# Kernel tuning notes

Measured on AMD Instinct MI355X. Metric: run time of the kernel, lower is better.

The kernel has to match this reference:

```python
import jax, jax.numpy as jnp
import numpy as np

BUCKET_BINS = np.array([0, 1, 2, 3, 4, 5, 7, 8, 15, 16, 31, 32, 63, 64], dtype=np.int32)
MAX_WINDOW = 8  # args.span_maximum_length


def _span_index_table(L):
    # Static enumeration of all spans of width 1..MAX_WINDOW (stride-1 unfold).
    starts, ends = [], []
    for w in range(1, min(L, MAX_WINDOW) + 1):
        s = np.arange(0, L - w + 1)
        starts.append(s)
        ends.append(s + w)
    return (np.concatenate(starts).astype(np.int32),
            np.concatenate(ends).astype(np.int32))


def _bucket(width):
    # index of last bin with width >= bin value
    return jnp.searchsorted(jnp.asarray(BUCKET_BINS), width, side='right') - 1


def _fnn(h, W1, b1, W2, b2, W3, b3):
    # Linear->ReLU->(Dropout: eval identity)->Linear->ReLU->Linear->Softmax
    h = jax.nn.relu(h @ W1 + b1)
    h = jax.nn.relu(h @ W2 + b2)
    return jax.nn.softmax(h @ W3 + b3, axis=-1)


def setup_inputs() -> dict:
    key = jax.random.key(0)
    ks = jax.random.split(key, 16)
    B, L, D = 8, 256, 768
    H, WD, DD = 1024, 25, 25
    span_dim = 2 * D + WD          # 1561
    pair_dim = 2 * span_dim + DD   # 3147
    f = jnp.float32

    def g(k, shape, scale):
        return jax.random.normal(k, shape, dtype=f) * scale

    return {
        'x': g(ks[0], (B, L, D), 1.0),
        'width_emb': g(ks[1], (len(BUCKET_BINS), WD), 0.02),
        'dist_emb': g(ks[2], (len(BUCKET_BINS), DD), 0.02),
        'Ws1': g(ks[3], (span_dim, H), 0.02), 'bs1': jnp.zeros((H,), f),
        'Ws2': g(ks[4], (H, H), 0.02), 'bs2': jnp.zeros((H,), f),
        'Ws3': g(ks[5], (H, 3), 0.02), 'bs3': jnp.zeros((3,), f),
        'Wp1': g(ks[6], (pair_dim, H), 0.02), 'bp1': jnp.zeros((H,), f),
        'Wp2': g(ks[7], (H, H), 0.02), 'bp2': jnp.zeros((H,), f),
        'Wp3': g(ks[8], (H, 4), 0.02), 'bp3': jnp.zeros((4,), f),
        'nz': 64,
    }


def reference(x, width_emb, dist_emb, Ws1, bs1, Ws2, bs2, Ws3, bs3,
              Wp1, bp1, Wp2, bp2, Wp3, bp3, nz):
    B, L, D = x.shape
    starts_np, ends_np = _span_index_table(L)
    starts = jnp.asarray(starts_np)
    ends = jnp.asarray(ends_np)

    # ---- SpanRepresentation: [start token, end token, width bucket emb] ----
    w_emb = width_emb[_bucket(ends - starts)]                     # [S, WD]
    spans = jnp.concatenate([
        x[:, starts_np, :],                                       # [B,S,D]
        x[:, ends_np - 1, :],                                     # [B,S,D]
        jnp.broadcast_to(w_emb, (B,) + w_emb.shape),              # [B,S,WD]
    ], axis=-1)                                                   # [B,S,span_dim]

    # ---- span_fnn + PrunedTargetOpinion (top-k on aspect/opinion probs) ----
    span_prob = _fnn(spans, Ws1, bs1, Ws2, bs2, Ws3, bs3)         # [B,S,3]
    _, t_idx = jax.lax.top_k(span_prob[:, :, 1], nz)              # aspect  [B,nz]
    _, o_idx = jax.lax.top_k(span_prob[:, :, 2], nz)              # opinion [B,nz]

    # ---- PairRepresentation: all target x opinion pairs ----
    t_rep = jnp.take_along_axis(spans, t_idx[:, :, None], axis=1) # [B,nz,sd]
    o_rep = jnp.take_along_axis(spans, o_idx[:, :, None], axis=1)
    ta, tb = starts[t_idx], ends[t_idx]                           # [B,nz]
    oc, od = starts[o_idx], ends[o_idx]
    # min_distance(a,b,c,d) = min(|b-c|, |a-d|)
    dist = jnp.minimum(jnp.abs(tb[:, :, None] - oc[:, None, :]),
                       jnp.abs(ta[:, :, None] - od[:, None, :]))  # [B,nz,nz]
    d_emb = dist_emb[_bucket(dist)]                               # [B,nz,nz,DD]
    sd = spans.shape[-1]
    pairs = jnp.concatenate([
        jnp.broadcast_to(t_rep[:, :, None, :], (B, nz, nz, sd)),
        jnp.broadcast_to(o_rep[:, None, :, :], (B, nz, nz, sd)),
        d_emb,
    ], axis=-1).reshape(B, nz * nz, 2 * sd + d_emb.shape[-1])     # [B,nz^2,pair_dim]

    pair_prob = _fnn(pairs, Wp1, bp1, Wp2, bp2, Wp3, bp3)         # [B,nz^2,4]
    return span_prob, pair_prob
```

## Files before the change

### kernel.cpp

```cpp
#include <hip/hip_runtime.h>
#include <cstdint>
#include <cstddef>

#define BATCH 8
#define SEQ   256
#define DIM   768
#define NSPAN 2020
#define HID   1024
#define NZ    64

typedef unsigned short u16;
typedef unsigned int   u32;
typedef unsigned long long u64;

typedef __bf16 bf16x8 __attribute__((ext_vector_type(8)));
typedef float  f32x4  __attribute__((ext_vector_type(4)));

__device__ __forceinline__ u16 f2bf(float f) {
    union { float f; u32 u; } x; x.f = f;
    u32 r = x.u + 0x7fffu + ((x.u >> 16) & 1u);
    return (u16)(r >> 16);
}
__device__ __forceinline__ float bf2f(u16 b) {
    union { u32 u; float f; } x; x.u = ((u32)b) << 16;
    return x.f;
}
__device__ __forceinline__ void splitbf(float v, u16& h, u16& l) {
    h = f2bf(v);
    l = f2bf(v - bf2f(h));
}

__device__ __forceinline__ void gld_lds16(const void* g, void* l) {
    __builtin_amdgcn_global_load_lds(
        (const __attribute__((address_space(1))) unsigned int*)g,
        (__attribute__((address_space(3))) unsigned int*)l, 16, 0, 0);
}

__device__ __forceinline__ void span_decode(int s, int& start, int& end, int& w) {
    int off = 0;
#pragma unroll
    for (int wi = 1; wi <= 8; ++wi) {
        int cnt = SEQ - wi + 1;
        if (s < off + cnt) { w = wi; start = s - off; end = start + wi; return; }
        off += cnt;
    }
    w = 8; start = 0; end = 8;
}

__device__ __forceinline__ int dbucket(int d) {
    int b = 0;
    b += (d >= 1);  b += (d >= 2);  b += (d >= 3);  b += (d >= 4);
    b += (d >= 5);  b += (d >= 7);  b += (d >= 8);  b += (d >= 15);
    b += (d >= 16); b += (d >= 31); b += (d >= 32); b += (d >= 63);
    b += (d >= 64);
    return b;
}

__device__ __forceinline__ void xcd_map(int L, int sft, int& bx, int& by) {
    int grp = L >> (3 + sft);
    int rem = L & ((1 << (3 + sft)) - 1);
    bx = rem >> 3;
    by = (grp << 3) | (rem & 7);
}

__global__ __launch_bounds__(256) void k_prep(
    const float* __restrict__ x,  u16* __restrict__ xh,   u16* __restrict__ xl,
    const float* __restrict__ wemb, const float* __restrict__ demb,
    const float* __restrict__ Ws1, const float* __restrict__ bs1,
    const float* __restrict__ Wp1, const float* __restrict__ bp1,
    float* __restrict__ wtabS, float* __restrict__ wtabPt,
    float* __restrict__ wtabPo, float* __restrict__ dtab)
{
    int bid = blockIdx.x, tid = threadIdx.x;
    if (bid < 6144) {
        int i = bid * 256 + tid;
        u16 h, l; splitbf(x[i], h, l);
        xh[i] = h; xl[i] = l;
        return;
    }
    int t = bid - 6144;
    int row = t >> 2;
    int h = (t & 3) * 256 + tid;
    const int wb[8] = {1,2,3,4,5,5,6,7};
    if (row < 8) {
        int bk = wb[row];
        float acc = bs1[h];
        for (int j = 0; j < 25; ++j) acc = fmaf(wemb[bk*25+j], Ws1[(size_t)(1536+j)*HID + h], acc);
        wtabS[row*HID + h] = acc;
    } else if (row < 16) {
        int bk = wb[row-8];
        float acc = 0.f;
        for (int j = 0; j < 25; ++j) acc = fmaf(wemb[bk*25+j], Wp1[(size_t)(1536+j)*HID + h], acc);
        wtabPt[(row-8)*HID + h] = acc;
    } else if (row < 24) {
        int bk = wb[row-16];
        float acc = 0.f;
        for (int j = 0; j < 25; ++j) acc = fmaf(wemb[bk*25+j], Wp1[(size_t)(3097+j)*HID + h], acc);
        wtabPo[(row-16)*HID + h] = acc;
    } else {
        int tt = row - 24;
        float acc = bp1[h];
        for (int j = 0; j < 25; ++j) acc = fmaf(demb[tt*25+j], Wp1[(size_t)(3122+j)*HID + h], acc);
        dtab[tt*HID + h] = acc;
    }
}

__global__ __launch_bounds__(256) void k_transpose(
    const float* __restrict__ Ws1, u16* __restrict__ W1Th, u16* __restrict__ W1Tl,
    const float* __restrict__ Ws2, u16* __restrict__ W2Th, u16* __restrict__ W2Tl,
    const float* __restrict__ Wp2, u16* __restrict__ Wp2T,
    const float* __restrict__ Wp1, u16* __restrict__ Wp1T4)
{
    __shared__ float tile[32][33];
    const int bid = blockIdx.x, tid = threadIdx.x;
    const int tr = tid >> 3;
    const int tc4 = (tid & 7) * 4;
    int job, tk, tn, blk = 0;
    if (bid < 1536)      { job = 0; tk = bid % 24; tn = bid / 24; }
    else if (bid < 2560) { job = 1; int t = bid - 1536; tk = t & 31; tn = t >> 5; }
    else if (bid < 3584) { job = 2; int t = bid - 2560; tk = t & 31; tn = t >> 5; }
    else                 { job = 3; int t = bid - 3584; blk = t / 768; int r = t - blk * 768; tk = r % 24; tn = r / 24; }
    const int k0 = tk * 32, n0 = tn * 32;

    int k = k0 + tr;
    float4 v;
    if (job == 0) {
        const float* s = (n0 < 1024) ? (Ws1 + (size_t)k * HID + n0)
                                     : (Ws1 + (size_t)(768 + k) * HID + (n0 - 1024));
        v = *(const float4*)(s + tc4);
    } else if (job == 1) {
        v = *(const float4*)(Ws2 + (size_t)k * HID + n0 + tc4);
    } else if (job == 2) {
        v = *(const float4*)(Wp2 + (size_t)k * HID + n0 + tc4);
    } else {
        const int roff[4] = {0, 768, 1561, 2329};
        v = *(const float4*)(Wp1 + (size_t)(roff[blk] + k) * HID + n0 + tc4);
    }
    tile[tr][tc4+0] = v.x; tile[tr][tc4+1] = v.y;
    tile[tr][tc4+2] = v.z; tile[tr][tc4+3] = v.w;
    __syncthreads();

    int nn = n0 + tr;
    float w0 = tile[tc4+0][tr], w1 = tile[tc4+1][tr];
    float w2 = tile[tc4+2][tr], w3 = tile[tc4+3][tr];
    if (job == 0) {
        size_t d = (size_t)nn * 768 + k0 + tc4;
        u16 h0,l0,h1,l1,h2,l2,h3,l3;
        splitbf(w0,h0,l0); splitbf(w1,h1,l1); splitbf(w2,h2,l2); splitbf(w3,h3,l3);
        *(uint2*)(W1Th + d) = make_uint2((u32)h0 | ((u32)h1 << 16), (u32)h2 | ((u32)h3 << 16));
        *(uint2*)(W1Tl + d) = make_uint2((u32)l0 | ((u32)l1 << 16), (u32)l2 | ((u32)l3 << 16));
    } else if (job == 1) {
        size_t d = (size_t)nn * 1024 + k0 + tc4;
        u16 h0,l0,h1,l1,h2,l2,h3,l3;
        splitbf(w0,h0,l0); splitbf(w1,h1,l1); splitbf(w2,h2,l2); splitbf(w3,h3,l3);
        *(uint2*)(W2Th + d) = make_uint2((u32)h0 | ((u32)h1 << 16), (u32)h2 | ((u32)h3 << 16));
        *(uint2*)(W2Tl + d) = make_uint2((u32)l0 | ((u32)l1 << 16), (u32)l2 | ((u32)l3 << 16));
    } else if (job == 2) {
        size_t d = (size_t)nn * 1024 + k0 + tc4;
        *(uint2*)(Wp2T + d) = make_uint2((u32)f2bf(w0) | ((u32)f2bf(w1) << 16),
                                         (u32)f2bf(w2) | ((u32)f2bf(w3) << 16));
    } else {
        size_t d = (size_t)blk * 786432 + (size_t)nn * 768 + k0 + tc4;
        *(uint2*)(Wp1T4 + d) = make_uint2((u32)f2bf(w0) | ((u32)f2bf(w1) << 16),
                                          (u32)f2bf(w2) | ((u32)f2bf(w3) << 16));
    }
}

__global__ __launch_bounds__(256) void k_gemm3bf(
    const u16* __restrict__ Ah, const u16* __restrict__ Al, int lda,
    const u16* __restrict__ BTh, const u16* __restrict__ BTl, int ldb,
    float* __restrict__ C, int ldc,
    int M, int K, int nby, int sft)
{
    int bx, by;
    xcd_map(blockIdx.x, sft, bx, by);
    if (by >= nby) return;
    __shared__ __align__(16) u16 sm[4 * 128 * 32];
    u16* sAh = sm;
    u16* sAl = sm + 4096;
    u16* sBh = sm + 8192;
    u16* sBl = sm + 12288;
    const int tid = threadIdx.x;
    const int bm = by * 128, bn = bx * 128;
    const int wave = tid >> 6, lane = tid & 63;
    const int wr = wave >> 1, wc = wave & 1;
    const int q = lane >> 4, tl = lane & 15;

    f32x4 zero = {0.f, 0.f, 0.f, 0.f};
    f32x4 acc[4][4];
#pragma unroll
    for (int i = 0; i < 4; ++i)
#pragma unroll
        for (int j = 0; j < 4; ++j) acc[i][j] = zero;

    const int srow = lane >> 2;
    const int scol = (lane & 3) * 8;
    int ra0 = bm + wave * 32 + srow;      if (ra0 >= M) ra0 = M - 1;
    int ra1 = bm + wave * 32 + 16 + srow; if (ra1 >= M) ra1 = M - 1;
    const int rb0 = bn + wave * 32 + srow;
    const int rb1 = bn + wave * 32 + 16 + srow;
    u16* dA0 = sAh + wave * 1024;  u16* dA1 = dA0 + 512;
    u16* dL0 = sAl + wave * 1024;  u16* dL1 = dL0 + 512;
    u16* dB0 = sBh + wave * 1024;  u16* dB1 = dB0 + 512;
    u16* dC0 = sBl + wave * 1024;  u16* dC1 = dC0 + 512;
    const u16* gA0 = Ah  + (size_t)ra0 * lda + scol;
    const u16* gA1 = Ah  + (size_t)ra1 * lda + scol;
    const u16* gL0 = Al  + (size_t)ra0 * lda + scol;
    const u16* gL1 = Al  + (size_t)ra1 * lda + scol;
    const u16* gB0 = BTh + (size_t)rb0 * ldb + scol;
    const u16* gB1 = BTh + (size_t)rb1 * ldb + scol;
    const u16* gC0 = BTl + (size_t)rb0 * ldb + scol;
    const u16* gC1 = BTl + (size_t)rb1 * ldb + scol;

    for (int k0 = 0; k0 < K; k0 += 32) {
        gld_lds16(gA0 + k0, dA0);
        gld_lds16(gA1 + k0, dA1);
        gld_lds16(gL0 + k0, dL0);
        gld_lds16(gL1 + k0, dL1);
        gld_lds16(gB0 + k0, dB0);
        gld_lds16(gB1 + k0, dB1);
        gld_lds16(gC0 + k0, dC0);
        gld_lds16(gC1 + k0, dC1);
        __syncthreads();
        bf16x8 ah[4], al[4], bh[4], bl[4];
#pragma unroll
        for (int t = 0; t < 4; ++t) {
            int arow = (wr*64 + t*16 + tl) * 32 + q*8;
            int brow = (wc*64 + t*16 + tl) * 32 + q*8;
            ah[t] = *(const bf16x8*)(&sAh[arow]);
            al[t] = *(const bf16x8*)(&sAl[arow]);
            bh[t] = *(const bf16x8*)(&sBh[brow]);
            bl[t] = *(const bf16x8*)(&sBl[brow]);
        }
#pragma unroll
        for (int ti = 0; ti < 4; ++ti)
#pragma unroll
            for (int tj = 0; tj < 4; ++tj) {
                acc[ti][tj] = __builtin_amdgcn_mfma_f32_16x16x32_bf16(ah[ti], bh[tj], acc[ti][tj], 0, 0, 0);
                acc[ti][tj] = __builtin_amdgcn_mfma_f32_16x16x32_bf16(al[ti], bh[tj], acc[ti][tj], 0, 0, 0);
                acc[ti][tj] = __builtin_amdgcn_mfma_f32_16x16x32_bf16(ah[ti], bl[tj], acc[ti][tj], 0, 0, 0);
            }
        __syncthreads();
    }
#pragma unroll
    for (int ti = 0; ti < 4; ++ti) {
#pragma unroll
        for (int tj = 0; tj < 4; ++tj) {
            int gcol = bn + wc*64 + tj*16 + tl;
#pragma unroll
            for (int r = 0; r < 4; ++r) {
                int grow = bm + wr*64 + ti*16 + q*4 + r;
                if (grow >= M) continue;
                C[(size_t)grow * ldc + gcol] = acc[ti][tj][r];
            }
        }
    }
}

__global__ __launch_bounds__(256) void k_span_l2(
    const u16* __restrict__ Ah, const u16* __restrict__ Al,
    const u16* __restrict__ BTh, const u16* __restrict__ BTl,
    const float* __restrict__ bs2, const float* __restrict__ Ws3,
    float* __restrict__ part, int M)
{
    int bx, by;
    xcd_map(blockIdx.x, 3, bx, by);
    if (by >= 127) return;
    __shared__ __align__(16) u16 sm[4 * 128 * 32];
    u16* sAh = sm;
    u16* sAl = sm + 4096;
    u16* sBh = sm + 8192;
    u16* sBl = sm + 12288;
    const int tid = threadIdx.x;
    const int bm = by * 128, bn = bx * 128;
    const int wave = tid >> 6, lane = tid & 63;
    const int wr = wave >> 1, wc = wave & 1;
    const int q = lane >> 4, tl = lane & 15;

    f32x4 zero = {0.f, 0.f, 0.f, 0.f};
    f32x4 acc[4][4];
#pragma unroll
    for (int i = 0; i < 4; ++i)
#pragma unroll
        for (int j = 0; j < 4; ++j) acc[i][j] = zero;

    const int srow = lane >> 2;
    const int scol = (lane & 3) * 8;
    int ra0 = bm + wave * 32 + srow;      if (ra0 >= M) ra0 = M - 1;
    int ra1 = bm + wave * 32 + 16 + srow; if (ra1 >= M) ra1 = M - 1;
    const int rb0 = bn + wave * 32 + srow;
    const int rb1 = bn + wave * 32 + 16 + srow;
    u16* dA0 = sAh + wave * 1024;  u16* dA1 = dA0 + 512;
    u16* dL0 = sAl + wave * 1024;  u16* dL1 = dL0 + 512;
    u16* dB0 = sBh + wave * 1024;  u16* dB1 = dB0 + 512;
    u16* dC0 = sBl + wave * 1024;  u16* dC1 = dC0 + 512;
    const u16* gA0 = Ah  + (size_t)ra0 * HID + scol;
    const u16* gA1 = Ah  + (size_t)ra1 * HID + scol;
    const u16* gL0 = Al  + (size_t)ra0 * HID + scol;
    const u16* gL1 = Al  + (size_t)ra1 * HID + scol;
    const u16* gB0 = BTh + (size_t)rb0 * HID + scol;
    const u16* gB1 = BTh + (size_t)rb1 * HID + scol;
    const u16* gC0 = BTl + (size_t)rb0 * HID + scol;
    const u16* gC1 = BTl + (size_t)rb1 * HID + scol;

    for (int k0 = 0; k0 < HID; k0 += 32) {
        gld_lds16(gA0 + k0, dA0);
        gld_lds16(gA1 + k0, dA1);
        gld_lds16(gL0 + k0, dL0);
        gld_lds16(gL1 + k0, dL1);
        gld_lds16(gB0 + k0, dB0);
        gld_lds16(gB1 + k0, dB1);
        gld_lds16(gC0 + k0, dC0);
        gld_lds16(gC1 + k0, dC1);
        __syncthreads();
        bf16x8 ah[4], al[4], bh[4], bl[4];
#pragma unroll
        for (int t = 0; t < 4; ++t) {
            int arow = (wr*64 + t*16 + tl) * 32 + q*8;
            int brow = (wc*64 + t*16 + tl) * 32 + q*8;
            ah[t] = *(const bf16x8*)(&sAh[arow]);
            al[t] = *(const bf16x8*)(&sAl[arow]);
            bh[t] = *(const bf16x8*)(&sBh[brow]);
            bl[t] = *(const bf16x8*)(&sBl[brow]);
        }
#pragma unroll
        for (int ti = 0; ti < 4; ++ti)
#pragma unroll
            for (int tj = 0; tj < 4; ++tj) {
                acc[ti][tj] = __builtin_amdgcn_mfma_f32_16x16x32_bf16(ah[ti], bh[tj], acc[ti][tj], 0, 0, 0);
                acc[ti][tj] = __builtin_amdgcn_mfma_f32_16x16x32_bf16(al[ti], bh[tj], acc[ti][tj], 0, 0, 0);
                acc[ti][tj] = __builtin_amdgcn_mfma_f32_16x16x32_bf16(ah[ti], bl[tj], acc[ti][tj], 0, 0, 0);
            }
        __syncthreads();
    }
    const int slot = bx * 2 + wc;
#pragma unroll
    for (int ti = 0; ti < 4; ++ti) {
#pragma unroll
        for (int r = 0; r < 4; ++r) {
            int grow = bm + wr*64 + ti*16 + q*4 + r;
            float l0 = 0.f, l1 = 0.f, l2 = 0.f;
#pragma unroll
            for (int tj = 0; tj < 4; ++tj) {
                int gcol = bn + wc*64 + tj*16 + tl;
                float v = fmaxf(acc[ti][tj][r] + bs2[gcol], 0.f);
                const float* w3 = Ws3 + gcol * 3;
                l0 = fmaf(v, w3[0], l0);
                l1 = fmaf(v, w3[1], l1);
                l2 = fmaf(v, w3[2], l2);
            }
#pragma unroll
            for (int off = 8; off > 0; off >>= 1) {
                l0 += __shfl_down(l0, off, 16);
                l1 += __shfl_down(l1, off, 16);
                l2 += __shfl_down(l2, off, 16);
            }
            if (tl == 0 && grow < M) {
                float* dst = part + ((size_t)grow * 16 + slot) * 3;
                dst[0] = l0; dst[1] = l1; dst[2] = l2;
            }
        }
    }
}

__global__ __launch_bounds__(256) void k_span_red(
    const float* __restrict__ part, const float* __restrict__ bs3,
    float* __restrict__ out)
{
    int r = blockIdx.x * 256 + threadIdx.x;
    if (r >= 16160) return;
    const float* p = part + (size_t)r * 48;
    float s0 = bs3[0], s1 = bs3[1], s2 = bs3[2];
#pragma unroll
    for (int t = 0; t < 16; ++t) {
        s0 += p[t*3]; s1 += p[t*3+1]; s2 += p[t*3+2];
    }
    float m = fmaxf(s0, fmaxf(s1, s2));
    float e0 = expf(s0 - m), e1 = expf(s1 - m), e2 = expf(s2 - m);
    float inv = 1.f / (e0 + e1 + e2);
    float* o = out + (size_t)r * 3;
    o[0] = e0 * inv; o[1] = e1 * inv; o[2] = e2 * inv;
}

__global__ __launch_bounds__(256) void k_pairL1(
    const u16* __restrict__ xh, const u16* __restrict__ Wp1T4,
    float* __restrict__ TO, const int* __restrict__ toks)
{
    __shared__ __align__(16) u16 sm[2 * 64 * 32];
    u16* sA = sm;
    u16* sB = sm + 2048;
    const int tid = threadIdx.x;
    const int bx = blockIdx.x & 15, by = blockIdx.x >> 4;
    const int bm = by * 64, bn = bx * 64;
    const int wave = tid >> 6, lane = tid & 63;
    const int wr = wave >> 1, wc = wave & 1;
    const int q = lane >> 4, tl = lane & 15;
    const bool isO = bm >= 512;

    f32x4 zero = {0.f, 0.f, 0.f, 0.f};
    f32x4 acc[2][2];
#pragma unroll
    for (int i = 0; i < 2; ++i)
#pragma unroll
        for (int j = 0; j < 2; ++j) acc[i][j] = zero;

    const int srow = tid >> 2;
    const int scol = (tid & 3) * 8;
    u16* dA = sA + wave * 512;
    u16* dB = sB + wave * 512;

#pragma unroll
    for (int p = 0; p < 2; ++p) {
        int arow = toks[bm + srow + p * 1024];
        const u16* gA = xh + (size_t)arow * DIM + scol;
        const u16* gB = Wp1T4 + ((size_t)((isO ? 2 : 0) + p) * 1024 + bn + srow) * DIM + scol;
        for (int k0 = 0; k0 < DIM; k0 += 32) {
            gld_lds16(gA + k0, dA);
            gld_lds16(gB + k0, dB);
            __syncthreads();
            bf16x8 af[2], bf[2];
#pragma unroll
            for (int t = 0; t < 2; ++t) {
                af[t] = *(const bf16x8*)(&sA[(wr*32 + t*16 + tl) * 32 + q*8]);
                bf[t] = *(const bf16x8*)(&sB[(wc*32 + t*16 + tl) * 32 + q*8]);
            }
#pragma unroll
            for (int ti = 0; ti < 2; ++ti)
#pragma unroll
                for (int tj = 0; tj < 2; ++tj)
                    acc[ti][tj] = __builtin_amdgcn_mfma_f32_16x16x32_bf16(af[ti], bf[tj], acc[ti][tj], 0, 0, 0);
            __syncthreads();
        }
    }
#pragma unroll
    for (int ti = 0; ti < 2; ++ti) {
#pragma unroll
        for (int tj = 0; tj < 2; ++tj) {
            int gcol = bn + wc*32 + tj*16 + tl;
#pragma unroll
            for (int r = 0; r < 4; ++r) {
                int grow = bm + wr*32 + ti*16 + q*4 + r;
                TO[(size_t)grow * HID + gcol] = acc[ti][tj][r];
            }
        }
    }
}

__global__ __launch_bounds__(256) void k_build_h1s(
    const float* __restrict__ XALL, const float* __restrict__ wtabS,
    u16* __restrict__ h1h, u16* __restrict__ h1l)
{
    int r = blockIdx.x;
    int b = r / NSPAN, s = r - b * NSPAN;
    int st, en, w; span_decode(s, st, en, w);
    const float4* xs = (const float4*)(XALL + (size_t)(b*SEQ + st) * 2048);
    const float4* xe = (const float4*)(XALL + (size_t)(b*SEQ + en - 1) * 2048 + 1024);
    const float4* wt = (const float4*)(wtabS + (size_t)(w-1) * HID);
    int t = threadIdx.x;
    float4 a = xs[t], bz = xe[t], c = wt[t];
    float v0 = fmaxf(a.x + bz.x + c.x, 0.f);
    float v1 = fmaxf(a.y + bz.y + c.y, 0.f);
    float v2 = fmaxf(a.z + bz.z + c.z, 0.f);
    float v3 = fmaxf(a.w + bz.w + c.w, 0.f);
    u16 h0,l0,h1,l1,h2,l2,h3,l3;
    splitbf(v0,h0,l0); splitbf(v1,h1,l1); splitbf(v2,h2,l2); splitbf(v3,h3,l3);
    size_t base = (size_t)r * HID + t * 4;
    *(uint2*)(h1h + base) = make_uint2((u32)h0 | ((u32)h1 << 16), (u32)h2 | ((u32)h3 << 16));
    *(uint2*)(h1l + base) = make_uint2((u32)l0 | ((u32)l1 << 16), (u32)l2 | ((u32)l3 << 16));
}

__global__ __launch_bounds__(256) void k_topk(
    const float* __restrict__ sp, int* __restrict__ t_idx, int* __restrict__ o_idx,
    int* __restrict__ toks)
{
    int b = blockIdx.x >> 1;
    int head = 1 + (blockIdx.x & 1);
    int* outp = (head == 1 ? t_idx : o_idx) + b * NZ;
    __shared__ u64 keys[2048];
    int tid = threadIdx.x;
#pragma unroll
    for (int ii = 0; ii < 8; ++ii) {
        int s = tid + ii * 256;
        u32 fb = 0;
        if (s < NSPAN) {
            union { float f; u32 u; } x;
            x.f = sp[((size_t)b * NSPAN + s) * 3 + head];
            fb = x.u;
        }
        keys[s] = ((u64)fb << 32) | (u64)(0xFFFFFFFFu - (u32)s);
    }
    __syncthreads();
    for (int k = 2; k <= 2048; k <<= 1) {
        for (int j = k >> 1; j > 0; j >>= 1) {
#pragma unroll
            for (int ii = 0; ii < 8; ++ii) {
                int i = tid + ii * 256;
                int ixj = i ^ j;
                if (ixj > i) {
                    u64 a = keys[i], c = keys[ixj];
                    bool desc = (i & k) == 0;
                    bool wrong = desc ? (a < c) : (a > c);
                    if (wrong) { keys[i] = c; keys[ixj] = a; }
                }
            }
            __syncthreads();
        }
    }
    if (tid < NZ) {
        u64 key = keys[tid];
        int fi = (int)(0xFFFFFFFFu - (u32)(key & 0xFFFFFFFFu));
        if (fi < 0 || fi >= NSPAN) fi = 0;
        outp[tid] = fi;
        int st, en, w; span_decode(fi, st, en, w);
        int base = (head == 1 ? 0 : 512) + b * NZ + tid;
        toks[base] = b * SEQ + st;
        toks[1024 + base] = b * SEQ + en - 1;
    }
}

__global__ __launch_bounds__(256) void k_build_h1p(
    const float* __restrict__ TO, const int* __restrict__ t_idx, const int* __restrict__ o_idx,
    const float* __restrict__ wtabPt, const float* __restrict__ wtabPo,
    const float* __restrict__ dtab, u16* __restrict__ h1p)
{
    int row = blockIdx.x;
    int b = row >> 12, i = (row >> 6) & 63, j = row & 63;
    int ts = t_idx[b*64 + i], os = o_idx[b*64 + j];
    int ta, tb, wt, oc, od, wo;
    span_decode(ts, ta, tb, wt);
    span_decode(os, oc, od, wo);
    int d1 = tb - oc; d1 = d1 < 0 ? -d1 : d1;
    int d2 = ta - od; d2 = d2 < 0 ? -d2 : d2;
    int dist = d1 < d2 ? d1 : d2;
    int db = dbucket(dist);
    const float4* T4 = (const float4*)(TO + (size_t)(b*64 + i) * HID);
    const float4* O4 = (const float4*)(TO + (size_t)(512 + b*64 + j) * HID);
    const float4* P4 = (const float4*)(wtabPt + (size_t)(wt-1) * HID);
    const float4* Q4 = (const float4*)(wtabPo + (size_t)(wo-1) * HID);
    const float4* D4 = (const float4*)(dtab + (size_t)db * HID);
    int t = threadIdx.x;
    float4 a = T4[t], c = O4[t], p = P4[t], q = Q4[t], d = D4[t];
    float vx = fmaxf(a.x + c.x + p.x + q.x + d.x, 0.f);
    float vy = fmaxf(a.y + c.y + p.y + q.y + d.y, 0.f);
    float vz = fmaxf(a.z + c.z + p.z + q.z + d.z, 0.f);
    float vw = fmaxf(a.w + c.w + p.w + q.w + d.w, 0.f);
    u32 p0 = (u32)f2bf(vx) | ((u32)f2bf(vy) << 16);
    u32 p1 = (u32)f2bf(vz) | ((u32)f2bf(vw) << 16);
    *(uint2*)(h1p + (size_t)row * HID + t * 4) = make_uint2(p0, p1);
}

__global__ __launch_bounds__(256) void k_pair_l2(
    const u16* __restrict__ Abf, const u16* __restrict__ BT,
    const float* __restrict__ bp2, const float* __restrict__ Wp3,
    float* __restrict__ part)
{
    int bx, by;
    xcd_map(blockIdx.x, 3, bx, by);
    __shared__ __align__(16) u16 sm[2 * 128 * 32];
    u16* As = sm;
    u16* Bs = sm + 4096;
    const int tid = threadIdx.x;
    const int bm = by * 128, bn = bx * 128;
    const int wave = tid >> 6, lane = tid & 63;
    const int wr = wave >> 1, wc = wave & 1;
    const int q = lane >> 4, tl = lane & 15;

    f32x4 zero = {0.f, 0.f, 0.f, 0.f};
    f32x4 acc[4][4];
#pragma unroll
    for (int i = 0; i < 4; ++i)
#pragma unroll
        for (int j = 0; j < 4; ++j) acc[i][j] = zero;

    const int srow = lane >> 2;
    const int scol = (lane & 3) * 8;
    const u16* gA0 = Abf + (size_t)(bm + wave*32 + srow) * 1024 + scol;
    const u16* gA1 = Abf + (size_t)(bm + wave*32 + 16 + srow) * 1024 + scol;
    const u16* gB0 = BT  + (size_t)(bn + wave*32 + srow) * 1024 + scol;
    const u16* gB1 = BT  + (size_t)(bn + wave*32 + 16 + srow) * 1024 + scol;
    u16* dA0 = As + wave * 1024;  u16* dA1 = dA0 + 512;
    u16* dB0 = Bs + wave * 1024;  u16* dB1 = dB0 + 512;

    for (int k0 = 0; k0 < 1024; k0 += 32) {
        gld_lds16(gA0 + k0, dA0);
        gld_lds16(gA1 + k0, dA1);
        gld_lds16(gB0 + k0, dB0);
        gld_lds16(gB1 + k0, dB1);
        __syncthreads();
        bf16x8 af[4], bf[4];
#pragma unroll
        for (int t = 0; t < 4; ++t) {
            af[t] = *(const bf16x8*)(&As[(wr*64 + t*16 + tl) * 32 + q*8]);
            bf[t] = *(const bf16x8*)(&Bs[(wc*64 + t*16 + tl) * 32 + q*8]);
        }
#pragma unroll
        for (int ti = 0; ti < 4; ++ti)
#pragma unroll
            for (int tj = 0; tj < 4; ++tj)
                acc[ti][tj] = __builtin_amdgcn_mfma_f32_16x16x32_bf16(af[ti], bf[tj], acc[ti][tj], 0, 0, 0);
        __syncthreads();
    }
    const int slot = bx * 2 + wc;
#pragma unroll
    for (int ti = 0; ti < 4; ++ti) {
#pragma unroll
        for (int r = 0; r < 4; ++r) {
            int grow = bm + wr*64 + ti*16 + q*4 + r;
            float l0 = 0.f, l1 = 0.f, l2 = 0.f, l3 = 0.f;
#pragma unroll
            for (int tj = 0; tj < 4; ++tj) {
                int gcol = bn + wc*64 + tj*16 + tl;
                float v = fmaxf(acc[ti][tj][r] + bp2[gcol], 0.f);
                const float4 w = *(const float4*)(Wp3 + gcol * 4);
                l0 = fmaf(v, w.x, l0); l1 = fmaf(v, w.y, l1);
                l2 = fmaf(v, w.z, l2); l3 = fmaf(v, w.w, l3);
            }
#pragma unroll
            for (int off = 8; off > 0; off >>= 1) {
                l0 += __shfl_down(l0, off, 16);
                l1 += __shfl_down(l1, off, 16);
                l2 += __shfl_down(l2, off, 16);
                l3 += __shfl_down(l3, off, 16);
            }
            if (tl == 0) {
                float* dst = part + ((size_t)grow * 16 + slot) * 4;
                dst[0] = l0; dst[1] = l1; dst[2] = l2; dst[3] = l3;
            }
        }
    }
}

__global__ __launch_bounds__(256) void k_pair_red(
    const float* __restrict__ part, const float* __restrict__ bp3,
    float* __restrict__ out)
{
    int r = blockIdx.x * 256 + threadIdx.x;
    const float4* p = (const float4*)(part + (size_t)r * 64);
    float s0 = bp3[0], s1 = bp3[1], s2 = bp3[2], s3 = bp3[3];
#pragma unroll
    for (int t = 0; t < 16; ++t) {
        float4 v = p[t];
        s0 += v.x; s1 += v.y; s2 += v.z; s3 += v.w;
    }
    float m = fmaxf(fmaxf(s0, s1), fmaxf(s2, s3));
    float e0 = expf(s0 - m), e1 = expf(s1 - m), e2 = expf(s2 - m), e3 = expf(s3 - m);
    float inv = 1.f / (e0 + e1 + e2 + e3);
    float* o = out + (size_t)r * 4;
    o[0] = e0 * inv; o[1] = e1 * inv; o[2] = e2 * inv; o[3] = e3 * inv;
}

extern "C" void kernel_launch(void* const* d_in, const int* in_sizes, int n_in,
                              void* d_out, int out_size, void* d_ws, size_t ws_size,
                              hipStream_t stream)
{
    const float* x    = (const float*)d_in[0];
    const float* wemb = (const float*)d_in[1];
    const float* demb = (const float*)d_in[2];
    const float* Ws1  = (const float*)d_in[3];
    const float* bs1  = (const float*)d_in[4];
    const float* Ws2  = (const float*)d_in[5];
    const float* bs2  = (const float*)d_in[6];
    const float* Ws3  = (const float*)d_in[7];
    const float* bs3  = (const float*)d_in[8];
    const float* Wp1  = (const float*)d_in[9];
    const float* bp1  = (const float*)d_in[10];
    const float* Wp2  = (const float*)d_in[11];
    const float* bp2  = (const float*)d_in[12];
    const float* Wp3  = (const float*)d_in[13];
    const float* bp3  = (const float*)d_in[14];
    float* out = (float*)d_out;
    char* ws = (char*)d_ws;

    const size_t RSZ = (size_t)32768 * HID * 2;
    size_t off = 0;
    auto alloc = [&](size_t bytes) -> void* {
        void* p = ws + off;
        off += (bytes + 255) & ~(size_t)255;
        return p;
    };
    char* R1 = (char*)alloc(RSZ);
    char* R2 = (char*)alloc(RSZ);
    u16*   h1h  = (u16*)R1;
    u16*   h1l  = (u16*)(R1 + (size_t)16160 * HID * 2);
    float* XALL = (float*)R2;
    u16*   xl   = (u16*)(R2 + (16u << 20));
    u16*   W1Th = (u16*)(R2 + (19u << 20));
    u16*   W1Tl = (u16*)(R2 + (22u << 20));
    u16*   h1p  = (u16*)R2;
    u16*   xh     = (u16*)alloc((size_t)2048 * DIM * 2);
    float* TO     = (float*)alloc((size_t)1024 * HID * 4);
    float* partS  = (float*)alloc((size_t)16160 * 16 * 3 * 4);
    float* partP  = (float*)alloc((size_t)32768 * 16 * 4 * 4);
    u16*   W2Th   = (u16*)alloc((size_t)1024 * 1024 * 2);
    u16*   W2Tl   = (u16*)alloc((size_t)1024 * 1024 * 2);
    u16*   Wp2T   = (u16*)alloc((size_t)1024 * 1024 * 2);
    u16*   Wp1T4  = (u16*)alloc((size_t)4 * 1024 * 768 * 2);
    float* wtabS  = (float*)alloc(8 * HID * 4);
    float* wtabPt = (float*)alloc(8 * HID * 4);
    float* wtabPo = (float*)alloc(8 * HID * 4);
    float* dtab   = (float*)alloc(14 * HID * 4);
    int*   t_idx  = (int*)alloc(BATCH * NZ * 4);
    int*   o_idx  = (int*)alloc(BATCH * NZ * 4);
    int*   toks   = (int*)alloc(2048 * 4);
    (void)ws_size; (void)in_sizes; (void)n_in; (void)out_size;

    k_prep<<<6296, 256, 0, stream>>>(x, xh, xl, wemb, demb, Ws1, bs1, Wp1, bp1,
                                     wtabS, wtabPt, wtabPo, dtab);
    k_transpose<<<6656, 256, 0, stream>>>(Ws1, W1Th, W1Tl, Ws2, W2Th, W2Tl,
                                          Wp2, Wp2T, Wp1, Wp1T4);

    k_gemm3bf<<<256, 256, 0, stream>>>(xh, xl, 768, W1Th, W1Tl, 768,
                                       XALL, 2048, 2048, 768, 16, 4);
    k_build_h1s<<<16160, 256, 0, stream>>>(XALL, wtabS, h1h, h1l);
    k_span_l2<<<1024, 256, 0, stream>>>(h1h, h1l, W2Th, W2Tl, bs2, Ws3, partS, 16160);
    k_span_red<<<64, 256, 0, stream>>>(partS, bs3, out);
    k_topk<<<16, 256, 0, stream>>>(out, t_idx, o_idx, toks);
    k_pairL1<<<256, 256, 0, stream>>>(xh, Wp1T4, TO, toks);
    k_build_h1p<<<32768, 256, 0, stream>>>(TO, t_idx, o_idx, wtabPt, wtabPo, dtab, h1p);
    k_pair_l2<<<2048, 256, 0, stream>>>(h1p, Wp2T, bp2, Wp3, partP);
    k_pair_red<<<128, 256, 0, stream>>>(partP, bp3, out + 48480);
}
```

Baseline: 471.8 us.

## Merge prep and transpose kernels, fold span softmax into top-k, split pairL1 K

```diff
diff --git a/kernel.cpp b/kernel.cpp
--- a/kernel.cpp
+++ b/kernel.cpp
@@ -66,60 +66,58 @@
 __global__ __launch_bounds__(256) void k_prep(
     const float* __restrict__ x,  u16* __restrict__ xh,   u16* __restrict__ xl,
     const float* __restrict__ wemb, const float* __restrict__ demb,
-    const float* __restrict__ Ws1, const float* __restrict__ bs1,
-    const float* __restrict__ Wp1, const float* __restrict__ bp1,
+    const float* __restrict__ bs1, const float* __restrict__ bp1,
     float* __restrict__ wtabS, float* __restrict__ wtabPt,
-    float* __restrict__ wtabPo, float* __restrict__ dtab)
-{
-    int bid = blockIdx.x, tid = threadIdx.x;
+    float* __restrict__ wtabPo, float* __restrict__ dtab,
+    const float* __restrict__ Ws1, u16* __restrict__ W1Th, u16* __restrict__ W1Tl,
+    const float* __restrict__ Ws2, u16* __restrict__ W2Th, u16* __restrict__ W2Tl,
+    const float* __restrict__ Wp2, u16* __restrict__ Wp2T,
+    const float* __restrict__ Wp1, u16* __restrict__ Wp1T4)
+{
+    __shared__ float tile[32][33];
+    const int bid = blockIdx.x, tid = threadIdx.x;
     if (bid < 6144) {
         int i = bid * 256 + tid;
         u16 h, l; splitbf(x[i], h, l);
         xh[i] = h; xl[i] = l;
         return;
     }
-    int t = bid - 6144;
-    int row = t >> 2;
-    int h = (t & 3) * 256 + tid;
-    const int wb[8] = {1,2,3,4,5,5,6,7};
-    if (row < 8) {
-        int bk = wb[row];
-        float acc = bs1[h];
-        for (int j = 0; j < 25; ++j) acc = fmaf(wemb[bk*25+j], Ws1[(size_t)(1536+j)*HID + h], acc);
-        wtabS[row*HID + h] = acc;
-    } else if (row < 16) {
-        int bk = wb[row-8];
-        float acc = 0.f;
-        for (int j = 0; j < 25; ++j) acc = fmaf(wemb[bk*25+j], Wp1[(size_t)(1536+j)*HID + h], acc);
-        wtabPt[(row-8)*HID + h] = acc;
-    } else if (row < 24) {
-        int bk = wb[row-16];
-        float acc = 0.f;
-        for (int j = 0; j < 25; ++j) acc = fmaf(wemb[bk*25+j], Wp1[(size_t)(3097+j)*HID + h], acc);
-        wtabPo[(row-16)*HID + h] = acc;
-    } else {
-        int tt = row - 24;
-        float acc = bp1[h];
-        for (int j = 0; j < 25; ++j) acc = fmaf(demb[tt*25+j], Wp1[(size_t)(3122+j)*HID + h], acc);
-        dtab[tt*HID + h] = acc;
-    }
-}
-
-__global__ __launch_bounds__(256) void k_transpose(
-    const float* __restrict__ Ws1, u16* __restrict__ W1Th, u16* __restrict__ W1Tl,
-    const float* __restrict__ Ws2, u16* __restrict__ W2Th, u16* __restrict__ W2Tl,
-    const float* __restrict__ Wp2, u16* __restrict__ Wp2T,
-    const float* __restrict__ Wp1, u16* __restrict__ Wp1T4)
-{
-    __shared__ float tile[32][33];
-    const int bid = blockIdx.x, tid = threadIdx.x;
+    if (bid < 6296) {
+        int t = bid - 6144;
+        int row = t >> 2;
+        int h = (t & 3) * 256 + tid;
+        const int wb[8] = {1,2,3,4,5,5,6,7};
+        if (row < 8) {
+            int bk = wb[row];
+            float acc = bs1[h];
+            for (int j = 0; j < 25; ++j) acc = fmaf(wemb[bk*25+j], Ws1[(size_t)(1536+j)*HID + h], acc);
+            wtabS[row*HID + h] = acc;
+        } else if (row < 16) {
+            int bk = wb[row-8];
+            float acc = 0.f;
+            for (int j = 0; j < 25; ++j) acc = fmaf(wemb[bk*25+j], Wp1[(size_t)(1536+j)*HID + h], acc);
+            wtabPt[(row-8)*HID + h] = acc;
+        } else if (row < 24) {
+            int bk = wb[row-16];
+            float acc = 0.f;
+            for (int j = 0; j < 25; ++j) acc = fmaf(wemb[bk*25+j], Wp1[(size_t)(3097+j)*HID + h], acc);
+            wtabPo[(row-16)*HID + h] = acc;
+        } else {
+            int tt = row - 24;
+            float acc = bp1[h];
+            for (int j = 0; j < 25; ++j) acc = fmaf(demb[tt*25+j], Wp1[(size_t)(3122+j)*HID + h], acc);
+            dtab[tt*HID + h] = acc;
+        }
+        return;
+    }
+    const int tb = bid - 6296;
     const int tr = tid >> 3;
     const int tc4 = (tid & 7) * 4;
     int job, tk, tn, blk = 0;
-    if (bid < 1536)      { job = 0; tk = bid % 24; tn = bid / 24; }
-    else if (bid < 2560) { job = 1; int t = bid - 1536; tk = t & 31; tn = t >> 5; }
-    else if (bid < 3584) { job = 2; int t = bid - 2560; tk = t & 31; tn = t >> 5; }
-    else                 { job = 3; int t = bid - 3584; blk = t / 768; int r = t - blk * 768; tk = r % 24; tn = r / 24; }
+    if (tb < 1536)      { job = 0; tk = tb % 24; tn = tb / 24; }
+    else if (tb < 2560) { job = 1; int t = tb - 1536; tk = t & 31; tn = t >> 5; }
+    else if (tb < 3584) { job = 2; int t = tb - 2560; tk = t & 31; tn = t >> 5; }
+    else                { job = 3; int t = tb - 3584; blk = t / 768; int r = t - blk * 768; tk = r % 24; tn = r / 24; }
     const int k0 = tk * 32, n0 = tn * 32;
 
     int k = k0 + tr;
@@ -363,34 +361,17 @@
     }
 }
 
-__global__ __launch_bounds__(256) void k_span_red(
-    const float* __restrict__ part, const float* __restrict__ bs3,
-    float* __restrict__ out)
-{
-    int r = blockIdx.x * 256 + threadIdx.x;
-    if (r >= 16160) return;
-    const float* p = part + (size_t)r * 48;
-    float s0 = bs3[0], s1 = bs3[1], s2 = bs3[2];
-#pragma unroll
-    for (int t = 0; t < 16; ++t) {
-        s0 += p[t*3]; s1 += p[t*3+1]; s2 += p[t*3+2];
-    }
-    float m = fmaxf(s0, fmaxf(s1, s2));
-    float e0 = expf(s0 - m), e1 = expf(s1 - m), e2 = expf(s2 - m);
-    float inv = 1.f / (e0 + e1 + e2);
-    float* o = out + (size_t)r * 3;
-    o[0] = e0 * inv; o[1] = e1 * inv; o[2] = e2 * inv;
-}
-
 __global__ __launch_bounds__(256) void k_pairL1(
     const u16* __restrict__ xh, const u16* __restrict__ Wp1T4,
-    float* __restrict__ TO, const int* __restrict__ toks)
+    float* __restrict__ TO2, const int* __restrict__ toks)
 {
     __shared__ __align__(16) u16 sm[2 * 64 * 32];
     u16* sA = sm;
     u16* sB = sm + 2048;
     const int tid = threadIdx.x;
-    const int bx = blockIdx.x & 15, by = blockIdx.x >> 4;
+    const int bid = blockIdx.x;
+    const int p = bid >> 8;
+    const int bx = bid & 15, by = (bid >> 4) & 15;
     const int bm = by * 64, bn = bx * 64;
     const int wave = tid >> 6, lane = tid & 63;
     const int wr = wave >> 1, wc = wave & 1;
@@ -409,29 +390,27 @@
     u16* dA = sA + wave * 512;
     u16* dB = sB + wave * 512;
 
-#pragma unroll
-    for (int p = 0; p < 2; ++p) {
-        int arow = toks[bm + srow + p * 1024];
-        const u16* gA = xh + (size_t)arow * DIM + scol;
-        const u16* gB = Wp1T4 + ((size_t)((isO ? 2 : 0) + p) * 1024 + bn + srow) * DIM + scol;
-        for (int k0 = 0; k0 < DIM; k0 += 32) {
-            gld_lds16(gA + k0, dA);
-            gld_lds16(gB + k0, dB);
-            __syncthreads();
-            bf16x8 af[2], bf[2];
-#pragma unroll
-            for (int t = 0; t < 2; ++t) {
-                af[t] = *(const bf16x8*)(&sA[(wr*32 + t*16 + tl) * 32 + q*8]);
-                bf[t] = *(const bf16x8*)(&sB[(wc*32 + t*16 + tl) * 32 + q*8]);
-            }
-#pragma unroll
-            for (int ti = 0; ti < 2; ++ti)
-#pragma unroll
-                for (int tj = 0; tj < 2; ++tj)
-                    acc[ti][tj] = __builtin_amdgcn_mfma_f32_16x16x32_bf16(af[ti], bf[tj], acc[ti][tj], 0, 0, 0);
-            __syncthreads();
-        }
-    }
+    int arow = toks[bm + srow + p * 1024];
+    const u16* gA = xh + (size_t)arow * DIM + scol;
+    const u16* gB = Wp1T4 + ((size_t)((isO ? 2 : 0) + p) * 1024 + bn + srow) * DIM + scol;
+    for (int k0 = 0; k0 < DIM; k0 += 32) {
+        gld_lds16(gA + k0, dA);
+        gld_lds16(gB + k0, dB);
+        __syncthreads();
+        bf16x8 af[2], bf[2];
+#pragma unroll
+        for (int t = 0; t < 2; ++t) {
+            af[t] = *(const bf16x8*)(&sA[(wr*32 + t*16 + tl) * 32 + q*8]);
+            bf[t] = *(const bf16x8*)(&sB[(wc*32 + t*16 + tl) * 32 + q*8]);
+        }
+#pragma unroll
+        for (int ti = 0; ti < 2; ++ti)
+#pragma unroll
+            for (int tj = 0; tj < 2; ++tj)
+                acc[ti][tj] = __builtin_amdgcn_mfma_f32_16x16x32_bf16(af[ti], bf[tj], acc[ti][tj], 0, 0, 0);
+        __syncthreads();
+    }
+    float* dstb = TO2 + (size_t)p * 1024 * HID;
 #pragma unroll
     for (int ti = 0; ti < 2; ++ti) {
 #pragma unroll
@@ -440,7 +419,7 @@
 #pragma unroll
             for (int r = 0; r < 4; ++r) {
                 int grow = bm + wr*32 + ti*16 + q*4 + r;
-                TO[(size_t)grow * HID + gcol] = acc[ti][tj][r];
+                dstb[(size_t)grow * HID + gcol] = acc[ti][tj][r];
             }
         }
     }
@@ -470,7 +449,8 @@
 }
 
 __global__ __launch_bounds__(256) void k_topk(
-    const float* __restrict__ sp, int* __restrict__ t_idx, int* __restrict__ o_idx,
+    const float* __restrict__ partS, const float* __restrict__ bs3,
+    float* __restrict__ out, int* __restrict__ t_idx, int* __restrict__ o_idx,
     int* __restrict__ toks)
 {
     int b = blockIdx.x >> 1;
@@ -483,8 +463,20 @@
         int s = tid + ii * 256;
         u32 fb = 0;
         if (s < NSPAN) {
+            const float* p = partS + (size_t)(b * NSPAN + s) * 48;
+            float s0 = bs3[0], s1 = bs3[1], s2 = bs3[2];
+#pragma unroll
+            for (int t = 0; t < 16; ++t) {
+                s0 += p[t*3]; s1 += p[t*3+1]; s2 += p[t*3+2];
+            }
+            float m = fmaxf(s0, fmaxf(s1, s2));
+            float e0 = expf(s0 - m), e1 = expf(s1 - m), e2 = expf(s2 - m);
+            float inv = 1.f / (e0 + e1 + e2);
+            float p0 = e0 * inv, p1 = e1 * inv, p2 = e2 * inv;
+            float* o = out + (size_t)(b * NSPAN + s) * 3;
+            o[0] = p0; o[1] = p1; o[2] = p2;
             union { float f; u32 u; } x;
-            x.f = sp[((size_t)b * NSPAN + s) * 3 + head];
+            x.f = (head == 1) ? p1 : p2;
             fb = x.u;
         }
         keys[s] = ((u64)fb << 32) | (u64)(0xFFFFFFFFu - (u32)s);
@@ -519,7 +511,7 @@
 }
 
 __global__ __launch_bounds__(256) void k_build_h1p(
-    const float* __restrict__ TO, const int* __restrict__ t_idx, const int* __restrict__ o_idx,
+    const float* __restrict__ TO2, const int* __restrict__ t_idx, const int* __restrict__ o_idx,
     const float* __restrict__ wtabPt, const float* __restrict__ wtabPo,
     const float* __restrict__ dtab, u16* __restrict__ h1p)
 {
@@ -533,17 +525,21 @@
     int d2 = ta - od; d2 = d2 < 0 ? -d2 : d2;
     int dist = d1 < d2 ? d1 : d2;
     int db = dbucket(dist);
-    const float4* T4 = (const float4*)(TO + (size_t)(b*64 + i) * HID);
-    const float4* O4 = (const float4*)(TO + (size_t)(512 + b*64 + j) * HID);
+    const size_t PS = (size_t)1024 * HID;
+    const float4* T0 = (const float4*)(TO2 + (size_t)(b*64 + i) * HID);
+    const float4* T1 = (const float4*)(TO2 + PS + (size_t)(b*64 + i) * HID);
+    const float4* O0 = (const float4*)(TO2 + (size_t)(512 + b*64 + j) * HID);
+    const float4* O1 = (const float4*)(TO2 + PS + (size_t)(512 + b*64 + j) * HID);
     const float4* P4 = (const float4*)(wtabPt + (size_t)(wt-1) * HID);
     const float4* Q4 = (const float4*)(wtabPo + (size_t)(wo-1) * HID);
     const float4* D4 = (const float4*)(dtab + (size_t)db * HID);
     int t = threadIdx.x;
-    float4 a = T4[t], c = O4[t], p = P4[t], q = Q4[t], d = D4[t];
-    float vx = fmaxf(a.x + c.x + p.x + q.x + d.x, 0.f);
-    float vy = fmaxf(a.y + c.y + p.y + q.y + d.y, 0.f);
-    float vz = fmaxf(a.z + c.z + p.z + q.z + d.z, 0.f);
-    float vw = fmaxf(a.w + c.w + p.w + q.w + d.w, 0.f);
+    float4 a0 = T0[t], a1 = T1[t], c0 = O0[t], c1 = O1[t];
+    float4 p = P4[t], q = Q4[t], d = D4[t];
+    float vx = fmaxf(a0.x + a1.x + c0.x + c1.x + p.x + q.x + d.x, 0.f);
+    float vy = fmaxf(a0.y + a1.y + c0.y + c1.y + p.y + q.y + d.y, 0.f);
+    float vz = fmaxf(a0.z + a1.z + c0.z + c1.z + p.z + q.z + d.z, 0.f);
+    float vw = fmaxf(a0.w + a1.w + c0.w + c1.w + p.w + q.w + d.w, 0.f);
     u32 p0 = (u32)f2bf(vx) | ((u32)f2bf(vy) << 16);
     u32 p1 = (u32)f2bf(vz) | ((u32)f2bf(vw) << 16);
     *(uint2*)(h1p + (size_t)row * HID + t * 4) = make_uint2(p0, p1);
@@ -688,7 +684,7 @@
     u16*   W1Tl = (u16*)(R2 + (22u << 20));
     u16*   h1p  = (u16*)R2;
     u16*   xh     = (u16*)alloc((size_t)2048 * DIM * 2);
-    float* TO     = (float*)alloc((size_t)1024 * HID * 4);
+    float* TO2    = (float*)alloc((size_t)2 * 1024 * HID * 4);
     float* partS  = (float*)alloc((size_t)16160 * 16 * 3 * 4);
     float* partP  = (float*)alloc((size_t)32768 * 16 * 4 * 4);
     u16*   W2Th   = (u16*)alloc((size_t)1024 * 1024 * 2);
@@ -704,19 +700,18 @@
     int*   toks   = (int*)alloc(2048 * 4);
     (void)ws_size; (void)in_sizes; (void)n_in; (void)out_size;
 
-    k_prep<<<6296, 256, 0, stream>>>(x, xh, xl, wemb, demb, Ws1, bs1, Wp1, bp1,
-                                     wtabS, wtabPt, wtabPo, dtab);
-    k_transpose<<<6656, 256, 0, stream>>>(Ws1, W1Th, W1Tl, Ws2, W2Th, W2Tl,
-                                          Wp2, Wp2T, Wp1, Wp1T4);
+    k_prep<<<12952, 256, 0, stream>>>(x, xh, xl, wemb, demb, bs1, bp1,
+                                      wtabS, wtabPt, wtabPo, dtab,
+                                      Ws1, W1Th, W1Tl, Ws2, W2Th, W2Tl,
+                                      Wp2, Wp2T, Wp1, Wp1T4);
 
     k_gemm3bf<<<256, 256, 0, stream>>>(xh, xl, 768, W1Th, W1Tl, 768,
                                        XALL, 2048, 2048, 768, 16, 4);
     k_build_h1s<<<16160, 256, 0, stream>>>(XALL, wtabS, h1h, h1l);
     k_span_l2<<<1024, 256, 0, stream>>>(h1h, h1l, W2Th, W2Tl, bs2, Ws3, partS, 16160);
-    k_span_red<<<64, 256, 0, stream>>>(partS, bs3, out);
-    k_topk<<<16, 256, 0, stream>>>(out, t_idx, o_idx, toks);
-    k_pairL1<<<256, 256, 0, stream>>>(xh, Wp1T4, TO, toks);
-    k_build_h1p<<<32768, 256, 0, stream>>>(TO, t_idx, o_idx, wtabPt, wtabPo, dtab, h1p);
+    k_topk<<<16, 256, 0, stream>>>(partS, bs3, out, t_idx, o_idx, toks);
+    k_pairL1<<<512, 256, 0, stream>>>(xh, Wp1T4, TO2, toks);
+    k_build_h1p<<<32768, 256, 0, stream>>>(TO2, t_idx, o_idx, wtabPt, wtabPo, dtab, h1p);
     k_pair_l2<<<2048, 256, 0, stream>>>(h1p, Wp2T, bp2, Wp3, partP);
     k_pair_red<<<128, 256, 0, stream>>>(partP, bp3, out + 48480);
 }
```

New measurement: 469.9 us. About the same (-0.4%).
